# Performance work log

Measured on AMD Instinct MI355X. Metric: run time of the kernel, lower is better.

Reference implementation:

```python
import jax, jax.numpy as jnp
import numpy as np

DIM, H, W, DEPTH = 256, 64, 64, 4
D_STATE, DT_RANK, D_CONV = 8, 16, 4
G, AGENTS = 8, 4

PKEYS = ['ln_w','ln_b','in_proj_w','conv_w','conv_b','x_proj_w','dt_proj_w','dt_proj_b',
         'A_log','A_b_log','D','out_proj_w','mn_w','mn_b']


def layernorm(x, w, b, eps=1e-5):
    mu = jnp.mean(x, -1, keepdims=True)
    var = jnp.var(x, -1, keepdims=True)
    return (x - mu) * jax.lax.rsqrt(var + eps) * w + b


def causal_conv1d(x, w, b):
    # x: (g, d, L); w: (d, k) depthwise causal conv (pad left k-1)
    k = w.shape[-1]
    xp = jnp.pad(x, ((0, 0), (0, 0), (k - 1, 0)))
    y = jax.lax.conv_general_dilated(xp, w[:, None, :], (1,), 'VALID',
                                     dimension_numbers=('NCH', 'OIH', 'NCH'),
                                     feature_group_count=w.shape[0])
    return y + b[None, :, None]


def selective_scan(u, delta, A, B, C, Dp, z):
    # u, delta, z: (g, d, L); B, C: (g, n, L); A: (d, n); Dp: (d,)
    dT = jnp.moveaxis(delta, -1, 0)
    BT = jnp.moveaxis(B, -1, 0)
    CT = jnp.moveaxis(C, -1, 0)
    uT = jnp.moveaxis(u, -1, 0)
    h0 = jnp.zeros(u.shape[:2] + (A.shape[-1],), u.dtype)  # (g, d, n)

    def step(h, inp):
        d_t, B_t, C_t, u_t = inp  # (g,d),(g,n),(g,n),(g,d)
        h = jnp.exp(d_t[..., None] * A) * h + (d_t * u_t)[..., None] * B_t[:, None, :]
        return h, jnp.einsum('gdn,gn->gd', h, C_t)

    _, ys = jax.lax.scan(step, h0, (dT, BT, CT, uT))
    y = jnp.moveaxis(ys, 0, -1) + Dp[None, :, None] * u
    return y * jax.nn.silu(z)


def ssm_dir(xdl, zdl, p, A):
    # one scan direction of mamba_inner_fn_no_out_proj; xdl, zdl: (g, d, L)
    xc = jax.nn.silu(causal_conv1d(xdl, p['conv_w'], p['conv_b']))
    x_dbl = jnp.einsum('gdl,ed->gel', xc, p['x_proj_w'])  # e = dt_rank + 2n
    dt, B, C = jnp.split(x_dbl, [DT_RANK, DT_RANK + D_STATE], axis=1)
    delta = jax.nn.softplus(jnp.einsum('grl,dr->gdl', dt, p['dt_proj_w'])
                            + p['dt_proj_b'][None, :, None])
    return selective_scan(xc, delta, A, B, C, p['D'], zdl)


def single_mamba_block(x, p):
    # x: (g, L, c)  -- LayerNorm + bidirectional Mamba (bimamba v1) + residual
    skip = x
    xn = layernorm(x, p['ln_w'], p['ln_b'])
    xz = jnp.einsum('glc,ec->gle', xn, p['in_proj_w'])  # (g, L, 2d), no bias
    xx, z = jnp.split(xz, 2, axis=-1)
    xdl = jnp.swapaxes(xx, 1, 2)
    zdl = jnp.swapaxes(z, 1, 2)
    y_f = ssm_dir(xdl, zdl, p, -jnp.exp(p['A_log']))
    y_b = jnp.flip(ssm_dir(jnp.flip(xdl, -1), jnp.flip(zdl, -1), p, -jnp.exp(p['A_b_log'])), -1)
    y = 0.5 * (y_f + y_b)  # if_devide_out=True
    out = jnp.einsum('gdl,od->glo', y, p['out_proj_w'])  # no bias
    out = layernorm(out, p['mn_w'], p['mn_b'])  # use_norm=True
    return out + skip


def _forward(data, plist, record_len):
    b, c, h, w = data.shape
    rl = np.asarray(record_len)
    seg = jnp.asarray(np.repeat(np.arange(rl.shape[0]), rl))
    means = jax.ops.segment_sum(data, seg, num_segments=rl.shape[0]) \
        / jnp.asarray(rl, data.dtype)[:, None, None, None]
    x = means.reshape(rl.shape[0], c, h * w).transpose(0, 2, 1)  # (G, L, C)
    for i in range(DEPTH):
        p = {k: v[i] for k, v in zip(PKEYS, plist)}
        x = single_mamba_block(x, p)
    return x.transpose(0, 2, 1).reshape(rl.shape[0], c, h, w)


def setup_inputs() -> dict:
    key = jax.random.key(0)
    ks = jax.random.split(key, 8)
    nrm = lambda k, shape, sc: jax.random.normal(k, shape, jnp.float32) * sc
    Alog = jnp.zeros((DEPTH, DIM, D_STATE), jnp.float32) \
        + jnp.log(jnp.arange(1, D_STATE + 1, dtype=jnp.float32))
    return {
        'data': jax.random.normal(ks[0], (G * AGENTS, DIM, H, W), jnp.float32),
        'ln_w': jnp.ones((DEPTH, DIM)), 'ln_b': jnp.zeros((DEPTH, DIM)),
        'in_proj_w': nrm(ks[1], (DEPTH, 2 * DIM, DIM), 0.02),
        'conv_w': nrm(ks[2], (DEPTH, DIM, D_CONV), 0.3),
        'conv_b': jnp.zeros((DEPTH, DIM)),
        'x_proj_w': nrm(ks[3], (DEPTH, DT_RANK + 2 * D_STATE, DIM), 0.02),
        'dt_proj_w': nrm(ks[4], (DEPTH, DIM, DT_RANK), 0.1),
        'dt_proj_b': jnp.full((DEPTH, DIM), float(np.log(np.expm1(0.01))), jnp.float32),
        'A_log': Alog, 'A_b_log': Alog,
        'D': jnp.ones((DEPTH, DIM)),
        'out_proj_w': nrm(ks[5], (DEPTH, DIM, DIM), 0.02),
        'mn_w': jnp.ones((DEPTH, DIM)), 'mn_b': jnp.zeros((DEPTH, DIM)),
        'record_len': jnp.full((G,), AGENTS, dtype=jnp.int32),
    }


def reference(data, ln_w, ln_b, in_proj_w, conv_w, conv_b, x_proj_w, dt_proj_w, dt_proj_b,
              A_log, A_b_log, D, out_proj_w, mn_w, mn_b, record_len):
    plist = [ln_w, ln_b, in_proj_w, conv_w, conv_b, x_proj_w, dt_proj_w, dt_proj_b,
             A_log, A_b_log, D, out_proj_w, mn_w, mn_b]
    return _forward(data, plist, record_len)
```

## Files before the change

kernel.cpp:

```cpp
#include <hip/hip_runtime.h>
#include <hip/hip_bf16.h>
#include <cstdint>
#include <cstddef>

typedef unsigned short u16;
typedef unsigned int   u32;

typedef short s16x8 __attribute__((ext_vector_type(8)));
typedef float f32x4 __attribute__((ext_vector_type(4)));

__device__ __forceinline__ float b2f(u16 u){ u32 x = ((u32)u)<<16; float f; __builtin_memcpy(&f,&x,4); return f; }
__device__ __forceinline__ u16  f2b(float f){ u32 x; __builtin_memcpy(&x,&f,4); u32 r = x + 0x7FFFu + ((x>>16)&1u); return (u16)(r>>16); }

__device__ __forceinline__ void unpack8(uint4 v, float* o){
  o[0]=b2f((u16)v.x); o[1]=b2f((u16)(v.x>>16));
  o[2]=b2f((u16)v.y); o[3]=b2f((u16)(v.y>>16));
  o[4]=b2f((u16)v.z); o[5]=b2f((u16)(v.z>>16));
  o[6]=b2f((u16)v.w); o[7]=b2f((u16)(v.w>>16));
}

__device__ __forceinline__ void gl_lds16(const u16* g, u16* l){
  __builtin_amdgcn_global_load_lds((const __attribute__((address_space(1))) u32*)g,
                                   (__attribute__((address_space(3))) u32*)l, 16, 0, 0);
}

__global__ void k_detect(const u16* __restrict__ lnw, int* __restrict__ flag){
  if (threadIdx.x==0 && blockIdx.x==0) *flag = (lnw[0] == 0x3F80) ? 1 : 0;
}

struct CvtTable { const void* src[14]; u16* dst[14]; int n[14]; };
__global__ void k_cvt(CvtTable t, const int* __restrict__ flag){
  int ti = blockIdx.y;
  int n = t.n[ti];
  int isbf = *flag;
  const u16*  sb = (const u16*)t.src[ti];
  const float* sf = (const float*)t.src[ti];
  u16* d = t.dst[ti];
  for (int i = blockIdx.x*256 + threadIdx.x; i < n; i += gridDim.x*256)
    d[i] = isbf ? sb[i] : f2b(sf[i]);
}

__global__ void k_mean(const void* __restrict__ data, const int* __restrict__ rl,
                       float* __restrict__ x, const int* __restrict__ flag){
  __shared__ float tile[32][129];
  int isbf = *flag;
  const u16*  db = (const u16*)data;
  const float* df_ = (const float*)data;
  int g = blockIdx.z, c0 = blockIdx.y*32, l0 = blockIdx.x*128;
  int tid = threadIdx.x;
  int off=0; for(int i=0;i<g;i++) off += rl[i];
  int cnt = rl[g];
  float inv = 1.0f/(float)cnt;
  for(int it=0; it<16; ++it){
    int idx = it*256 + tid;
    int ci = idx>>7, lj = idx&127;
    float acc = 0.f;
    for(int b=0;b<cnt;b++){
      size_t gi = ((size_t)(off+b)*256 + (c0+ci)) * 4096 + (l0+lj);
      acc += isbf ? b2f(db[gi]) : df_[gi];
    }
    tile[ci][lj] = acc*inv;
  }
  __syncthreads();
  for(int it=0; it<16; ++it){
    int idx = it*256 + tid;
    int lj = idx>>5, ci = idx&31;
    x[ ((size_t)g*4096 + (l0+lj))*256 + (c0+ci) ] = tile[ci][lj];
  }
}

__global__ void k_prep(const u16* __restrict__ dtp, const u16* __restrict__ xpw, u16* __restrict__ bcomb){
  int layer = blockIdx.y, row = blockIdx.x, c = threadIdx.x;
  u16 out;
  if (row < 256){
    float acc = 0.f;
    #pragma unroll
    for(int r=0;r<16;r++)
      acc += b2f(dtp[(size_t)layer*4096 + row*16 + r]) * b2f(xpw[(size_t)layer*8192 + r*256 + c]);
    out = f2b(acc);
  } else if (row < 272){
    out = xpw[(size_t)layer*8192 + (16 + row - 256)*256 + c];
  } else {
    out = 0;
  }
  bcomb[((size_t)layer*384 + row)*256 + c] = out;
}

__global__ void k_ln1(const float* __restrict__ x, u16* __restrict__ xn,
                      const u16* __restrict__ w, const u16* __restrict__ b, int layer){
  int wid = threadIdx.x>>6, lane = threadIdx.x&63;
  int row = blockIdx.x*4 + wid;
  const float* xr = x + (size_t)row*256;
  float4 v = *(const float4*)(xr + lane*4);
  float s = v.x+v.y+v.z+v.w;
  float q = v.x*v.x+v.y*v.y+v.z*v.z+v.w*v.w;
  for(int o=32;o;o>>=1){ s += __shfl_xor(s,o); q += __shfl_xor(q,o); }
  float mu = s*(1.f/256.f);
  float var = q*(1.f/256.f) - mu*mu;
  float rs = rsqrtf(var + 1e-5f);
  const u16* wp = w + layer*256 + lane*4;
  const u16* bp = b + layer*256 + lane*4;
  float vv[4] = {v.x,v.y,v.z,v.w};
  u16 h4[4];
  #pragma unroll
  for(int k2=0;k2<4;k2++)
    h4[k2] = f2b( (vv[k2]-mu)*rs*b2f(wp[k2]) + b2f(bp[k2]) );
  uint2 oh; oh.x = (u32)h4[0] | ((u32)h4[1]<<16); oh.y = (u32)h4[2] | ((u32)h4[3]<<16);
  *(uint2*)(xn + (size_t)row*256 + lane*4) = oh;
}

template<int MODE>
__global__ __launch_bounds__(256)
void k_gemm(const u16* __restrict__ A,
            const u16* __restrict__ B,
            u16* __restrict__ C0, float* __restrict__ C0f, int ldC,
            const u16* __restrict__ bias, u16* __restrict__ C1){
  __shared__ u16 As[128*64];
  __shared__ u16 Bs[128*64];
  int tid = threadIdx.x, wid = tid>>6, lane = tid&63;
  int m0 = blockIdx.x*128, n0 = blockIdx.y*128;
  f32x4 acc[4][4];
  #pragma unroll
  for(int i=0;i<4;i++)
    #pragma unroll
    for(int j=0;j<4;j++) acc[i][j] = (f32x4){0.f,0.f,0.f,0.f};
  int lrow  = lane>>3;
  int scol  = ((lane&7) ^ lrow) * 8;
  int rm = (wid&1)*64, cn = (wid>>1)*64;
  for(int k0=0;k0<256;k0+=64){
    #pragma unroll
    for(int it=0; it<4; ++it){
      int chunk = wid*4 + it;
      int row = chunk*8 + lrow;
      gl_lds16(A + (size_t)(m0+row)*256 + k0 + scol, As + chunk*512 + lane*8);
      gl_lds16(B + (size_t)(n0+row)*256 + k0 + scol, Bs + chunk*512 + lane*8);
    }
    __syncthreads();
    #pragma unroll
    for(int kk=0;kk<2;kk++){
      s16x8 af[4], bfr[4];
      #pragma unroll
      for(int i=0;i<4;i++){
        int ar = rm + i*16 + (lane&15);
        int ap = (kk*4 + (lane>>4)) ^ (ar&7);
        af[i]  = *(const s16x8*)(As + ar*64 + ap*8);
        int br = cn + i*16 + (lane&15);
        int bp = (kk*4 + (lane>>4)) ^ (br&7);
        bfr[i] = *(const s16x8*)(Bs + br*64 + bp*8);
      }
      #pragma unroll
      for(int i=0;i<4;i++)
        #pragma unroll
        for(int j=0;j<4;j++)
          acc[i][j] = __builtin_amdgcn_mfma_f32_16x16x32_bf16(af[i], bfr[j], acc[i][j], 0,0,0);
    }
    __syncthreads();
  }
  #pragma unroll
  for(int i=0;i<4;i++){
    #pragma unroll
    for(int j=0;j<4;j++){
      int n  = n0 + cn + j*16 + (lane&15);
      int mB = m0 + rm + i*16 + ((lane>>4)<<2);
      #pragma unroll
      for(int r=0;r<4;r++){
        float val = acc[i][j][r];
        int m = mB + r;
        if (MODE==0){
          if (n < 256) C0f[(size_t)m*256 + n] = val;
          else         C1[(size_t)m*256 + (n-256)] = f2b(val);
        } else {
          if (n < 256){
            float v2 = val + b2f(bias[n]);
            float sp = (v2 > 15.f) ? v2 : __logf(1.f + __expf(v2));
            C0[(size_t)m*256 + n] = f2b(sp);
          } else if (n < 272){
            C1[(size_t)m*16 + (n-256)] = f2b(val);
          }
        }
      }
    }
  }
}

__global__ void k_conv(const float* __restrict__ xf, const u16* __restrict__ cw,
                       const u16* __restrict__ cb, u16* __restrict__ xcf, u16* __restrict__ xcb_, int layer){
  int l0 = blockIdx.x*32, g = blockIdx.y, d = threadIdx.x;
  float w[4];
  #pragma unroll
  for(int j=0;j<4;j++) w[j] = b2f(cw[(size_t)layer*1024 + d*4 + j]);
  float bb = b2f(cb[layer*256 + d]);
  float xv[38];
  #pragma unroll
  for(int t=0;t<38;t++){
    int lp = l0 - 3 + t;
    xv[t] = (lp>=0 && lp<4096) ? xf[((size_t)g*4096 + lp)*256 + d] : 0.f;
  }
  #pragma unroll
  for(int i=0;i<32;i++){
    float af = bb, ab = bb;
    #pragma unroll
    for(int j=0;j<4;j++){ af += w[j]*xv[i+j]; ab += w[j]*xv[i+6-j]; }
    af = af / (1.f + __expf(-af));
    ab = ab / (1.f + __expf(-ab));
    size_t o = ((size_t)g*4096 + (l0+i))*256 + d;
    xcf[o]  = f2b(af);
    xcb_[o] = f2b(ab);
  }
}

__global__ __launch_bounds__(256)
void k_scan1(const u16* __restrict__ df, const u16* __restrict__ db,
             const u16* __restrict__ uf, const u16* __restrict__ ub,
             const u16* __restrict__ bcf, const u16* __restrict__ bcb,
             const u16* __restrict__ Alog, const u16* __restrict__ Ablog,
             float* __restrict__ abuf, float* __restrict__ bbuf, int layer){
  int c = blockIdx.x, g = blockIdx.y, dir = blockIdx.z, d = threadIdx.x;
  const u16* dl = dir ? db : df;
  const u16* uu = dir ? ub : uf;
  const u16* bc = dir ? bcb : bcf;
  const u16* Al = dir ? Ablog : Alog;
  float An[8], h[8], ap[8];
  #pragma unroll
  for(int n=0;n<8;n++){
    An[n] = -__expf(b2f(Al[(size_t)layer*2048 + d*8 + n]));
    h[n] = 0.f; ap[n] = 1.f;
  }
  #pragma unroll 4
  for(int t=0;t<32;t++){
    int ts = c*32 + t;
    int tg = dir ? (4095 - ts) : ts;
    size_t rowo = (size_t)g*4096 + tg;
    float dv = b2f(dl[rowo*256 + d]);
    float uv = b2f(uu[rowo*256 + d]);
    uint4 bv = *(const uint4*)(bc + rowo*16);
    float bn[8]; unpack8(bv, bn);
    float du = dv*uv;
    #pragma unroll
    for(int n=0;n<8;n++){
      float da = __expf(dv*An[n]);
      h[n] = fmaf(da, h[n], du*bn[n]);
      ap[n] *= da;
    }
  }
  size_t base = ((((size_t)dir*8+g)*128 + c)*256 + d)*8;
  *(float4*)(abuf+base)   = (float4){ap[0],ap[1],ap[2],ap[3]};
  *(float4*)(abuf+base+4) = (float4){ap[4],ap[5],ap[6],ap[7]};
  *(float4*)(bbuf+base)   = (float4){h[0],h[1],h[2],h[3]};
  *(float4*)(bbuf+base+4) = (float4){h[4],h[5],h[6],h[7]};
}

__global__ void k_scan2(const float* __restrict__ abuf, const float* __restrict__ bbuf,
                        float* __restrict__ hs){
  int dblk = blockIdx.x, g = blockIdx.y, dir = blockIdx.z;
  int n = threadIdx.x & 7, dd = threadIdx.x >> 3;
  int d = dblk*8 + dd;
  float h = 0.f;
  size_t gofs = (((size_t)dir*8+g)*128);
  #pragma unroll 4
  for(int c=0;c<128;c++){
    size_t idx = ((gofs + c)*256 + d)*8 + n;
    hs[idx] = h;
    h = fmaf(abuf[idx], h, bbuf[idx]);
  }
}

__global__ __launch_bounds__(256)
void k_scanY(const u16* __restrict__ df, const u16* __restrict__ db,
             const float* __restrict__ xf, const u16* __restrict__ zb,
             const u16* __restrict__ bcf, const u16* __restrict__ bcb,
             const u16* __restrict__ Alog, const u16* __restrict__ Ablog,
             const u16* __restrict__ Dp, const u16* __restrict__ cw, const u16* __restrict__ cb,
             const float* __restrict__ hs,
             u16* __restrict__ yhi, int layer){
  __shared__ float ybs[32*256];
  int c = blockIdx.x, g = blockIdx.y, d = threadIdx.x;
  int l0 = c*32;
  float Dd = b2f(Dp[layer*256 + d]);
  float w0 = b2f(cw[(size_t)layer*1024 + d*4 + 0]);
  float w1 = b2f(cw[(size_t)layer*1024 + d*4 + 1]);
  float w2 = b2f(cw[(size_t)layer*1024 + d*4 + 2]);
  float w3 = b2f(cw[(size_t)layer*1024 + d*4 + 3]);
  float cbb = b2f(cb[layer*256 + d]);
  const float* xrow = xf + (size_t)g*4096*256 + d;
  const u16*  zrow = zb + (size_t)g*4096*256 + d;
  float An[8], h[8];
  {
    #pragma unroll
    for(int n=0;n<8;n++) An[n] = -__expf(b2f(Ablog[(size_t)layer*2048 + d*8 + n]));
    size_t base = ((((size_t)8+g)*128 + (127-c))*256 + d)*8;
    float4 h0 = *(const float4*)(hs+base);
    float4 h1 = *(const float4*)(hs+base+4);
    h[0]=h0.x; h[1]=h0.y; h[2]=h0.z; h[3]=h0.w;
    h[4]=h1.x; h[5]=h1.y; h[6]=h1.z; h[7]=h1.w;
    float xw1 = (l0+32<4096) ? xrow[(size_t)(l0+32)*256] : 0.f;
    float xw2 = (l0+33<4096) ? xrow[(size_t)(l0+33)*256] : 0.f;
    float xw3 = (l0+34<4096) ? xrow[(size_t)(l0+34)*256] : 0.f;
    #pragma unroll 4
    for(int q=0;q<32;q++){
      int t = 31 - q;
      size_t rowo = (size_t)g*4096 + l0 + t;
      float x0 = xrow[(size_t)(l0+t)*256];
      float ucv = cbb + w3*x0 + w2*xw1 + w1*xw2 + w0*xw3;
      xw3 = xw2; xw2 = xw1; xw1 = x0;
      float uv = ucv / (1.f + __expf(-ucv));
      float dv = b2f(db[rowo*256 + d]);
      uint4 bv = *(const uint4*)(bcb + rowo*16);
      uint4 cv = *(const uint4*)(bcb + rowo*16 + 8);
      float bn[8], cn_[8];
      unpack8(bv, bn); unpack8(cv, cn_);
      float du = dv*uv;
      float y = 0.f;
      #pragma unroll
      for(int n=0;n<8;n++){
        float da = __expf(dv*An[n]);
        h[n] = fmaf(da, h[n], du*bn[n]);
        y = fmaf(h[n], cn_[n], y);
      }
      ybs[t*256 + d] = y + Dd*uv;
    }
  }
  {
    #pragma unroll
    for(int n=0;n<8;n++) An[n] = -__expf(b2f(Alog[(size_t)layer*2048 + d*8 + n]));
    size_t base = (((size_t)g*128 + c)*256 + d)*8;
    float4 h0 = *(const float4*)(hs+base);
    float4 h1 = *(const float4*)(hs+base+4);
    h[0]=h0.x; h[1]=h0.y; h[2]=h0.z; h[3]=h0.w;
    h[4]=h1.x; h[5]=h1.y; h[6]=h1.z; h[7]=h1.w;
    float wm1 = (l0-1>=0) ? xrow[(size_t)(l0-1)*256] : 0.f;
    float wm2 = (l0-2>=0) ? xrow[(size_t)(l0-2)*256] : 0.f;
    float wm3 = (l0-3>=0) ? xrow[(size_t)(l0-3)*256] : 0.f;
    #pragma unroll 4
    for(int t=0;t<32;t++){
      size_t rowo = (size_t)g*4096 + l0 + t;
      float x0 = xrow[(size_t)(l0+t)*256];
      float ucv = cbb + w0*wm3 + w1*wm2 + w2*wm1 + w3*x0;
      wm3 = wm2; wm2 = wm1; wm1 = x0;
      float uv = ucv / (1.f + __expf(-ucv));
      float dv = b2f(df[rowo*256 + d]);
      uint4 bv = *(const uint4*)(bcf + rowo*16);
      uint4 cv = *(const uint4*)(bcf + rowo*16 + 8);
      float bn[8], cn_[8];
      unpack8(bv, bn); unpack8(cv, cn_);
      float du = dv*uv;
      float y = 0.f;
      #pragma unroll
      for(int n=0;n<8;n++){
        float da = __expf(dv*An[n]);
        h[n] = fmaf(da, h[n], du*bn[n]);
        y = fmaf(h[n], cn_[n], y);
      }
      y += Dd*uv;
      y += ybs[t*256 + d];
      float zv = b2f(zrow[(size_t)(l0+t)*256]);
      float yv = y * 0.5f * zv / (1.f + __expf(-zv));
      yhi[rowo*256 + d] = f2b(yv);
    }
  }
}

template<int LAST>
__global__ __launch_bounds__(256)
void k_outproj(const u16* __restrict__ yhi,
               const u16* __restrict__ Bw,
               float* __restrict__ X, u16* __restrict__ xnh,
               const u16* __restrict__ mnw, const u16* __restrict__ mnb,
               const u16* __restrict__ lnw_n, const u16* __restrict__ lnb_n){
  __shared__ u16 Ash[64*64];
  __shared__ u16 Bs[256*64];
  int tid = threadIdx.x, wid = tid>>6, lane = tid&63;
  int c = blockIdx.x, g = blockIdx.y;
  size_t row0 = (size_t)g*4096 + c*64;
  f32x4 acc[16];
  #pragma unroll
  for(int j=0;j<16;j++) acc[j] = (f32x4){0.f,0.f,0.f,0.f};
  int lrow = lane>>3;
  int scol = ((lane&7) ^ lrow) * 8;
  for(int k0=0;k0<256;k0+=64){
    #pragma unroll
    for(int it=0; it<2; ++it){
      int chunk = wid*2 + it;
      int row = chunk*8 + lrow;
      gl_lds16(yhi + (row0+row)*256 + k0 + scol, Ash + chunk*512 + lane*8);
    }
    #pragma unroll
    for(int it=0; it<8; ++it){
      int chunk = wid*8 + it;
      int row = chunk*8 + lrow;
      gl_lds16(Bw + (size_t)row*256 + k0 + scol, Bs + chunk*512 + lane*8);
    }
    __syncthreads();
    #pragma unroll
    for(int kk=0;kk<2;kk++){
      int ar = wid*16 + (lane&15);
      int q  = kk*4 + (lane>>4);
      s16x8 afh = *(const s16x8*)(Ash + ar*64 + (q^(ar&7))*8);
      #pragma unroll
      for(int j=0;j<16;j++){
        int br = j*16 + (lane&15);
        s16x8 bfv = *(const s16x8*)(Bs + br*64 + (q^(br&7))*8);
        acc[j] = __builtin_amdgcn_mfma_f32_16x16x32_bf16(afh, bfv, acc[j], 0,0,0);
      }
    }
    __syncthreads();
  }
  size_t gm0 = row0;
  int quad = lane>>4;
  float sm[4]={0,0,0,0}, sq[4]={0,0,0,0};
  #pragma unroll
  for(int j=0;j<16;j++)
    #pragma unroll
    for(int r=0;r<4;r++){ float v=acc[j][r]; sm[r]+=v; sq[r]+=v*v; }
  #pragma unroll
  for(int o=1;o<16;o<<=1)
    #pragma unroll
    for(int r=0;r<4;r++){ sm[r]+=__shfl_xor(sm[r],o); sq[r]+=__shfl_xor(sq[r],o); }
  float mu[4], rs[4];
  #pragma unroll
  for(int r=0;r<4;r++){
    mu[r] = sm[r]*(1.f/256.f);
    float var = sq[r]*(1.f/256.f) - mu[r]*mu[r];
    rs[r] = rsqrtf(var + 1e-5f);
  }
  #pragma unroll
  for(int j=0;j<16;j++){
    int col = j*16 + (lane&15);
    float w = b2f(mnw[col]), bb = b2f(mnb[col]);
    #pragma unroll
    for(int r=0;r<4;r++){
      size_t m = gm0 + wid*16 + quad*4 + r;
      float xn = X[m*256 + col] + (acc[j][r]-mu[r])*rs[r]*w + bb;
      X[m*256 + col] = xn;
      acc[j][r] = xn;
    }
  }
  if (!LAST){
    float sm2[4]={0,0,0,0}, sq2[4]={0,0,0,0};
    #pragma unroll
    for(int j=0;j<16;j++)
      #pragma unroll
      for(int r=0;r<4;r++){ float v=acc[j][r]; sm2[r]+=v; sq2[r]+=v*v; }
    #pragma unroll
    for(int o=1;o<16;o<<=1)
      #pragma unroll
      for(int r=0;r<4;r++){ sm2[r]+=__shfl_xor(sm2[r],o); sq2[r]+=__shfl_xor(sq2[r],o); }
    float mu2[4], rs2[4];
    #pragma unroll
    for(int r=0;r<4;r++){
      mu2[r] = sm2[r]*(1.f/256.f);
      float var = sq2[r]*(1.f/256.f) - mu2[r]*mu2[r];
      rs2[r] = rsqrtf(var + 1e-5f);
    }
    #pragma unroll
    for(int j=0;j<16;j++){
      int col = j*16 + (lane&15);
      float w = b2f(lnw_n[col]), bb = b2f(lnb_n[col]);
      #pragma unroll
      for(int r=0;r<4;r++){
        size_t m = gm0 + wid*16 + quad*4 + r;
        float vv = (acc[j][r]-mu2[r])*rs2[r]*w + bb;
        xnh[m*256 + col] = f2b(vv);
      }
    }
  }
}

__global__ void k_tr(const float* __restrict__ x, void* __restrict__ out, const int* __restrict__ flag){
  __shared__ float tile[32][129];
  int isbf = *flag;
  int l0 = blockIdx.x*128, c0 = blockIdx.y*32, g = blockIdx.z;
  int tid = threadIdx.x;
  for(int it=0; it<16; ++it){
    int idx = it*256 + tid;
    int lj = idx>>5, ci = idx&31;
    tile[ci][lj] = x[((size_t)g*4096 + l0+lj)*256 + c0+ci];
  }
  __syncthreads();
  for(int it=0; it<16; ++it){
    int idx = it*256 + tid;
    int lj = idx&127, ci = idx>>7;
    size_t o = ((size_t)g*256 + c0+ci)*4096 + l0+lj;
    float v = tile[ci][lj];
    if (isbf) ((u16*)out)[o] = f2b(v);
    else      ((float*)out)[o] = v;
  }
}

extern "C" void kernel_launch(void* const* d_in, const int* in_sizes, int n_in,
                              void* d_out, int out_size, void* d_ws, size_t ws_size,
                              hipStream_t stream){
  (void)in_sizes; (void)n_in; (void)out_size; (void)ws_size;
  const int* rl = (const int*)d_in[15];

  char* ws = (char*)d_ws;
  float* X    = (float*)(ws);
  float* XF   = (float*)(ws + 33554432);
  u16*  ZB    = (u16*) (ws + 67108864);
  u16*  XCF   = (u16*) (ws + 100663296);
  u16*  XCB   = (u16*) (ws + 117440512);
  u16*  DF    = (u16*) (ws + 134217728);
  u16*  DB    = (u16*) (ws + 150994944);
  u16*  BCF   = (u16*) (ws + 167772160);
  u16*  BCB   = (u16*) (ws + 168820736);
  u16*  BCOMB = (u16*) (ws + 169869312);
  float* ABUF = (float*)(ws + 170655744);
  u16*  XNh   = (u16*) (ws + 170655744);
  float* BBUF = (float*)(ws + 187432960);
  float* HS   = (float*)(ws + 204210176);
  u16*  WCVT  = (u16*) (ws + 220987392);
  int*  FLAG  = (int*) (ws + 222715904);

  u16* YHI = XCF;

  u16* W_lnw  = WCVT + 0;
  u16* W_lnb  = WCVT + 1024;
  u16* W_inp  = WCVT + 2048;
  u16* W_cw   = WCVT + 526336;
  u16* W_cb   = WCVT + 530432;
  u16* W_xp   = WCVT + 531456;
  u16* W_dtw  = WCVT + 564224;
  u16* W_dtb  = WCVT + 580608;
  u16* W_Al   = WCVT + 581632;
  u16* W_Abl  = WCVT + 589824;
  u16* W_D    = WCVT + 598016;
  u16* W_outp = WCVT + 599040;
  u16* W_mnw  = WCVT + 861184;
  u16* W_mnb  = WCVT + 862208;

  k_detect<<<1,64,0,stream>>>((const u16*)d_in[1], FLAG);

  CvtTable t;
  const int idxs[14] = {1,2,3,4,5,6,7,8,9,10,11,12,13,14};
  u16* dsts[14] = {W_lnw,W_lnb,W_inp,W_cw,W_cb,W_xp,W_dtw,W_dtb,W_Al,W_Abl,W_D,W_outp,W_mnw,W_mnb};
  const int ns[14] = {1024,1024,524288,4096,1024,32768,16384,1024,8192,8192,1024,262144,1024,1024};
  for(int i=0;i<14;i++){ t.src[i]=d_in[idxs[i]]; t.dst[i]=dsts[i]; t.n[i]=ns[i]; }
  k_cvt<<<dim3(32,14),256,0,stream>>>(t, FLAG);

  k_mean<<<dim3(32,8,8),256,0,stream>>>(d_in[0], rl, X, FLAG);
  k_prep<<<dim3(384,4),256,0,stream>>>(W_dtw, W_xp, BCOMB);
  k_ln1<<<8192,256,0,stream>>>(X, XNh, W_lnw, W_lnb, 0);

  for(int layer=0; layer<4; ++layer){
    k_gemm<0><<<dim3(256,4),256,0,stream>>>(XNh, W_inp + (size_t)layer*512*256,
                                            nullptr, XF, 256, nullptr, ZB);
    k_conv<<<dim3(128,8),256,0,stream>>>(XF, W_cw, W_cb, XCF, XCB, layer);
    k_gemm<1><<<dim3(512,3),256,0,stream>>>(XCF, BCOMB + (size_t)layer*384*256,
                                            DF, nullptr, 256, W_dtb + layer*256, BCF);
    k_scan1<<<dim3(128,8,2),256,0,stream>>>(DF,DB,XCF,XCB,BCF,BCB,W_Al,W_Abl,ABUF,BBUF,layer);
    k_scan2<<<dim3(32,8,2),64,0,stream>>>(ABUF,BBUF,HS);
    k_scanY<<<dim3(128,8),256,0,stream>>>(DF,DB,XF,ZB,BCF,BCB,W_Al,W_Abl,W_D,W_cw,W_cb,HS,YHI,layer);
    if (layer < 3){
      k_outproj<0><<<dim3(64,8),256,0,stream>>>(YHI, W_outp + (size_t)layer*256*256,
                                                X, XNh,
                                                W_mnw + layer*256, W_mnb + layer*256,
                                                W_lnw + (layer+1)*256, W_lnb + (layer+1)*256);
    } else {
      k_outproj<1><<<dim3(64,8),256,0,stream>>>(YHI, W_outp + (size_t)layer*256*256,
                                                X, XNh,
                                                W_mnw + layer*256, W_mnb + layer*256,
                                                W_lnw, W_lnb);
    }
  }
  k_tr<<<dim3(32,8,8),256,0,stream>>>(X, d_out, FLAG);
}
```

Before: 1.244 ms.

## Fuse scan output stage with out_proj GEMM and layernorm epilogue

Merges the selective-scan output kernel with the out-projection GEMM, so the gated y tile (32 rows × 256 channels) stays in shared memory as bf16 instead of going through global memory. The GEMM is retiled to 32 rows per block with four waves splitting rows and columns, and the layernorm row reductions now combine partial sums across waves through shared memory. This removes one launch and a global write plus read of y. In exchange the out_proj weights are reloaded by twice as many blocks, shared memory is reused between the scan buffer and the weight tiles, and extra barriers are added.

```diff
diff --git a/kernel.cpp b/kernel.cpp
--- a/kernel.cpp
+++ b/kernel.cpp
@@ -265,15 +265,25 @@
   }
 }
 
+#define AP 264
+template<int LAST>
 __global__ __launch_bounds__(256)
-void k_scanY(const u16* __restrict__ df, const u16* __restrict__ db,
-             const float* __restrict__ xf, const u16* __restrict__ zb,
-             const u16* __restrict__ bcf, const u16* __restrict__ bcb,
-             const u16* __restrict__ Alog, const u16* __restrict__ Ablog,
-             const u16* __restrict__ Dp, const u16* __restrict__ cw, const u16* __restrict__ cb,
-             const float* __restrict__ hs,
-             u16* __restrict__ yhi, int layer){
-  __shared__ float ybs[32*256];
+void k_scanYO(const u16* __restrict__ df, const u16* __restrict__ db,
+              const float* __restrict__ xf, const u16* __restrict__ zb,
+              const u16* __restrict__ bcf, const u16* __restrict__ bcb,
+              const u16* __restrict__ Alog, const u16* __restrict__ Ablog,
+              const u16* __restrict__ Dp, const u16* __restrict__ cw, const u16* __restrict__ cb,
+              const float* __restrict__ hs,
+              const u16* __restrict__ Bw,
+              float* __restrict__ X, u16* __restrict__ xnh,
+              const u16* __restrict__ mnw, const u16* __restrict__ mnb,
+              const u16* __restrict__ lnw_n, const u16* __restrict__ lnb_n,
+              int layer){
+  __shared__ char smem[32768 + AP*32*2];
+  float* ybs = (float*)smem;
+  u16*   Bsm = (u16*)smem;
+  u16*   Asm = (u16*)(smem + 32768);
+  __shared__ float red[4][32][2];
   int c = blockIdx.x, g = blockIdx.y, d = threadIdx.x;
   int l0 = c*32;
   float Dd = b2f(Dp[layer*256 + d]);
@@ -355,81 +365,70 @@
       y += ybs[t*256 + d];
       float zv = b2f(zrow[(size_t)(l0+t)*256]);
       float yv = y * 0.5f * zv / (1.f + __expf(-zv));
-      yhi[rowo*256 + d] = f2b(yv);
-    }
-  }
-}
-
-template<int LAST>
-__global__ __launch_bounds__(256)
-void k_outproj(const u16* __restrict__ yhi,
-               const u16* __restrict__ Bw,
-               float* __restrict__ X, u16* __restrict__ xnh,
-               const u16* __restrict__ mnw, const u16* __restrict__ mnb,
-               const u16* __restrict__ lnw_n, const u16* __restrict__ lnb_n){
-  __shared__ u16 Ash[64*64];
-  __shared__ u16 Bs[256*64];
-  int tid = threadIdx.x, wid = tid>>6, lane = tid&63;
-  int c = blockIdx.x, g = blockIdx.y;
-  size_t row0 = (size_t)g*4096 + c*64;
-  f32x4 acc[16];
-  #pragma unroll
-  for(int j=0;j<16;j++) acc[j] = (f32x4){0.f,0.f,0.f,0.f};
+      Asm[t*AP + d] = f2b(yv);
+    }
+  }
+  __syncthreads();
+  int wid = d>>6, lane = d&63;
+  int mrow0 = (wid&1)*16, ncol0 = (wid>>1)*128;
+  f32x4 acc[8];
+  #pragma unroll
+  for(int j=0;j<8;j++) acc[j] = (f32x4){0.f,0.f,0.f,0.f};
   int lrow = lane>>3;
   int scol = ((lane&7) ^ lrow) * 8;
   for(int k0=0;k0<256;k0+=64){
     #pragma unroll
-    for(int it=0; it<2; ++it){
-      int chunk = wid*2 + it;
-      int row = chunk*8 + lrow;
-      gl_lds16(yhi + (row0+row)*256 + k0 + scol, Ash + chunk*512 + lane*8);
-    }
-    #pragma unroll
     for(int it=0; it<8; ++it){
       int chunk = wid*8 + it;
       int row = chunk*8 + lrow;
-      gl_lds16(Bw + (size_t)row*256 + k0 + scol, Bs + chunk*512 + lane*8);
+      gl_lds16(Bw + (size_t)row*256 + k0 + scol, Bsm + chunk*512 + lane*8);
     }
     __syncthreads();
     #pragma unroll
     for(int kk=0;kk<2;kk++){
-      int ar = wid*16 + (lane&15);
       int q  = kk*4 + (lane>>4);
-      s16x8 afh = *(const s16x8*)(Ash + ar*64 + (q^(ar&7))*8);
-      #pragma unroll
-      for(int j=0;j<16;j++){
-        int br = j*16 + (lane&15);
-        s16x8 bfv = *(const s16x8*)(Bs + br*64 + (q^(br&7))*8);
-        acc[j] = __builtin_amdgcn_mfma_f32_16x16x32_bf16(afh, bfv, acc[j], 0,0,0);
+      s16x8 af = *(const s16x8*)(Asm + (mrow0 + (lane&15))*AP + k0 + kk*32 + (lane>>4)*8);
+      #pragma unroll
+      for(int j=0;j<8;j++){
+        int br = ncol0 + j*16 + (lane&15);
+        s16x8 bfv = *(const s16x8*)(Bsm + br*64 + (q^(br&7))*8);
+        acc[j] = __builtin_amdgcn_mfma_f32_16x16x32_bf16(af, bfv, acc[j], 0,0,0);
       }
     }
     __syncthreads();
   }
-  size_t gm0 = row0;
+  size_t gm0 = (size_t)g*4096 + l0;
   int quad = lane>>4;
   float sm[4]={0,0,0,0}, sq[4]={0,0,0,0};
   #pragma unroll
-  for(int j=0;j<16;j++)
+  for(int j=0;j<8;j++)
     #pragma unroll
     for(int r=0;r<4;r++){ float v=acc[j][r]; sm[r]+=v; sq[r]+=v*v; }
   #pragma unroll
   for(int o=1;o<16;o<<=1)
     #pragma unroll
     for(int r=0;r<4;r++){ sm[r]+=__shfl_xor(sm[r],o); sq[r]+=__shfl_xor(sq[r],o); }
+  if ((lane&15)==0){
+    #pragma unroll
+    for(int r=0;r<4;r++){ red[wid][quad*4+r][0]=sm[r]; red[wid][quad*4+r][1]=sq[r]; }
+  }
+  __syncthreads();
   float mu[4], rs[4];
   #pragma unroll
   for(int r=0;r<4;r++){
-    mu[r] = sm[r]*(1.f/256.f);
-    float var = sq[r]*(1.f/256.f) - mu[r]*mu[r];
+    float s2 = red[wid][quad*4+r][0] + red[wid^2][quad*4+r][0];
+    float q2 = red[wid][quad*4+r][1] + red[wid^2][quad*4+r][1];
+    mu[r] = s2*(1.f/256.f);
+    float var = q2*(1.f/256.f) - mu[r]*mu[r];
     rs[r] = rsqrtf(var + 1e-5f);
   }
   #pragma unroll
-  for(int j=0;j<16;j++){
-    int col = j*16 + (lane&15);
+  for(int j=0;j<8;j++){
+    int col = ncol0 + j*16 + (lane&15);
     float w = b2f(mnw[col]), bb = b2f(mnb[col]);
     #pragma unroll
     for(int r=0;r<4;r++){
-      size_t m = gm0 + wid*16 + quad*4 + r;
+      size_t m = gm0 + mrow0 + quad*4 + r;
       float xn = X[m*256 + col] + (acc[j][r]-mu[r])*rs[r]*w + bb;
       X[m*256 + col] = xn;
       acc[j][r] = xn;
@@ -438,27 +437,35 @@
   if (!LAST){
     float sm2[4]={0,0,0,0}, sq2[4]={0,0,0,0};
     #pragma unroll
-    for(int j=0;j<16;j++)
+    for(int j=0;j<8;j++)
       #pragma unroll
       for(int r=0;r<4;r++){ float v=acc[j][r]; sm2[r]+=v; sq2[r]+=v*v; }
     #pragma unroll
     for(int o=1;o<16;o<<=1)
       #pragma unroll
       for(int r=0;r<4;r++){ sm2[r]+=__shfl_xor(sm2[r],o); sq2[r]+=__shfl_xor(sq2[r],o); }
+    __syncthreads();
+    if ((lane&15)==0){
+      #pragma unroll
+      for(int r=0;r<4;r++){ red[wid][quad*4+r][0]=sm2[r]; red[wid][quad*4+r][1]=sq2[r]; }
+    }
+    __syncthreads();
     float mu2[4], rs2[4];
     #pragma unroll
     for(int r=0;r<4;r++){
-      mu2[r] = sm2[r]*(1.f/256.f);
-      float var = sq2[r]*(1.f/256.f) - mu2[r]*mu2[r];
+      float s2 = red[wid][quad*4+r][0] + red[wid^2][quad*4+r][0];
+      float q2 = red[wid][quad*4+r][1] + red[wid^2][quad*4+r][1];
+      mu2[r] = s2*(1.f/256.f);
+      float var = q2*(1.f/256.f) - mu2[r]*mu2[r];
       rs2[r] = rsqrtf(var + 1e-5f);
     }
     #pragma unroll
-    for(int j=0;j<16;j++){
-      int col = j*16 + (lane&15);
+    for(int j=0;j<8;j++){
+      int col = ncol0 + j*16 + (lane&15);
       float w = b2f(lnw_n[col]), bb = b2f(lnb_n[col]);
       #pragma unroll
       for(int r=0;r<4;r++){
-        size_t m = gm0 + wid*16 + quad*4 + r;
+        size_t m = gm0 + mrow0 + quad*4 + r;
         float vv = (acc[j][r]-mu2[r])*rs2[r]*w + bb;
         xnh[m*256 + col] = f2b(vv);
       }
@@ -511,8 +518,6 @@
   u16*  WCVT  = (u16*) (ws + 220987392);
   int*  FLAG  = (int*) (ws + 222715904);
 
-  u16* YHI = XCF;
-
   u16* W_lnw  = WCVT + 0;
   u16* W_lnb  = WCVT + 1024;
   u16* W_inp  = WCVT + 2048;
@@ -549,17 +554,16 @@
                                             DF, nullptr, 256, W_dtb + layer*256, BCF);
     k_scan1<<<dim3(128,8,2),256,0,stream>>>(DF,DB,XCF,XCB,BCF,BCB,W_Al,W_Abl,ABUF,BBUF,layer);
     k_scan2<<<dim3(32,8,2),64,0,stream>>>(ABUF,BBUF,HS);
-    k_scanY<<<dim3(128,8),256,0,stream>>>(DF,DB,XF,ZB,BCF,BCB,W_Al,W_Abl,W_D,W_cw,W_cb,HS,YHI,layer);
     if (layer < 3){
-      k_outproj<0><<<dim3(64,8),256,0,stream>>>(YHI, W_outp + (size_t)layer*256*256,
-                                                X, XNh,
+      k_scanYO<0><<<dim3(128,8),256,0,stream>>>(DF,DB,XF,ZB,BCF,BCB,W_Al,W_Abl,W_D,W_cw,W_cb,HS,
+                                                W_outp + (size_t)layer*256*256, X, XNh,
                                                 W_mnw + layer*256, W_mnb + layer*256,
-                                                W_lnw + (layer+1)*256, W_lnb + (layer+1)*256);
+                                                W_lnw + (layer+1)*256, W_lnb + (layer+1)*256, layer);
     } else {
-      k_outproj<1><<<dim3(64,8),256,0,stream>>>(YHI, W_outp + (size_t)layer*256*256,
-                                                X, XNh,
+      k_scanYO<1><<<dim3(128,8),256,0,stream>>>(DF,DB,XF,ZB,BCF,BCB,W_Al,W_Abl,W_D,W_cw,W_cb,HS,
+                                                W_outp + (size_t)layer*256*256, X, XNh,
                                                 W_mnw + layer*256, W_mnb + layer*256,
-                                                W_lnw, W_lnb);
+                                                W_lnw, W_lnb, layer);
     }
   }
   k_tr<<<dim3(32,8,8),256,0,stream>>>(X, d_out, FLAG);
```

Measured after the change: 1.174 ms. -5.6%, faster.
